# Kernel optimization log

Measured on AMD Instinct MI355X. Metric: run time of the kernel, lower is better.

Reference implementation:

```python
import jax, jax.numpy as jnp
import numpy as np


def _conv1x1(x, w, b):
    # x: [B,Cin,H,W], w: [Cout,Cin], b: [Cout]
    return jnp.einsum('bchw,oc->bohw', x, w) + b[None, :, None, None]


def setup_inputs() -> dict:
    key = jax.random.key(0)
    ks = jax.random.split(key, 9)
    C, Cb = 256, 128
    B, H, W = 8, 32, 32
    s_in = 1.0 / np.sqrt(C)
    s_bn = 1.0 / np.sqrt(Cb)
    return {
        'x': jax.random.normal(ks[0], (B, C, H, W), dtype=jnp.float32),
        'theta_w': jax.random.uniform(ks[1], (Cb, C), jnp.float32, -s_in, s_in),
        'theta_b': jax.random.uniform(ks[2], (Cb,), jnp.float32, -s_in, s_in),
        'phi_w': jax.random.uniform(ks[3], (Cb, C), jnp.float32, -s_in, s_in),
        'phi_b': jax.random.uniform(ks[4], (Cb,), jnp.float32, -s_in, s_in),
        'g_w': jax.random.uniform(ks[5], (Cb, C), jnp.float32, -s_in, s_in),
        'g_b': jax.random.uniform(ks[6], (Cb,), jnp.float32, -s_in, s_in),
        'W_w': jax.random.uniform(ks[7], (C, Cb), jnp.float32, -s_bn, s_bn),
        'W_b': jax.random.uniform(ks[8], (C,), jnp.float32, -s_bn, s_bn),
    }


def reference(x, theta_w, theta_b, phi_w, phi_b, g_w, g_b, W_w, W_b):
    B, C, H, Wd = x.shape
    Cb = theta_w.shape[0]
    theta = _conv1x1(x, theta_w, theta_b).reshape(-1, Cb)      # [N, Cb] (row-major, as torch)
    phi = _conv1x1(x, phi_w, phi_b).reshape(Cb, -1)            # [Cb, N]
    g = _conv1x1(x, g_w, g_b).reshape(-1, Cb)                  # [N, Cb]
    attn = jax.nn.softmax(theta @ phi, axis=1)                 # [N, N] global attention
    out = (attn @ g).reshape(B, -1, H, Wd)                     # [B, Cb, H, W]
    return _conv1x1(out, W_w, W_b) + x
```

## Files before the change

kernel.cpp:

```cpp
#include <hip/hip_runtime.h>

typedef unsigned short u16;
typedef __attribute__((ext_vector_type(8))) short short8;
typedef __attribute__((ext_vector_type(4))) float f32x4;

__device__ __forceinline__ u16 f2bf(float f){
  union { float f; unsigned u; } v; v.f = f;
  unsigned u = v.u;
  u += 0x7fffu + ((u >> 16) & 1u);
  return (u16)(u >> 16);
}
__device__ __forceinline__ float bf2f(u16 h){
  union { unsigned u; float f; } v; v.u = ((unsigned)h) << 16;
  return v.f;
}

__global__ __launch_bounds__(256) void wcast_kernel(
    const float* __restrict__ tw, const float* __restrict__ pw,
    const float* __restrict__ gw, u16* __restrict__ Wall)
{
  int i = blockIdx.x*256 + threadIdx.x;
  const float* src = (i < 8192) ? tw : (i < 16384) ? pw : gw;
  int off = (i & 8191) * 4;
  float4 v = *(const float4*)(src + off);
  ushort4 o;
  o.x = f2bf(v.x); o.y = f2bf(v.y); o.z = f2bf(v.z); o.w = f2bf(v.w);
  *(ushort4*)(Wall + (size_t)i*4) = o;
}

__global__ __launch_bounds__(256) void xcast_kernel(
    const float* __restrict__ x, u16* __restrict__ XT)
{
  __shared__ float tile[64][69];
  const int b = blockIdx.z, c0 = blockIdx.y*64, hw0 = blockIdx.x*64;
  const int t = threadIdx.x;
  {
    int r = t >> 2, cs = (t & 3) * 16;
    const float* s = x + (size_t)(b*256 + c0 + r)*1024 + hw0 + cs;
    #pragma unroll
    for (int i=0;i<4;i++)
      *(float4*)&tile[r][cs + i*4] = *(const float4*)(s + i*4);
  }
  __syncthreads();
  {
    int hr = t >> 2, cc = (t & 3) * 16;
    __align__(16) u16 tmp[16];
    #pragma unroll
    for (int i=0;i<16;i++) tmp[i] = f2bf(tile[cc + i][hr]);
    u16* d = XT + (size_t)(b*1024 + hw0 + hr)*256 + c0 + cc;
    *(uint4*)d     = *(uint4*)&tmp[0];
    *(uint4*)(d+8) = *(uint4*)&tmp[8];
  }
}

__global__ __launch_bounds__(256, 2) void proj_mfma_kernel(
    const u16* __restrict__ XT, const u16* __restrict__ Wall,
    const float* __restrict__ tb, const float* __restrict__ pb,
    const float* __restrict__ gb,
    u16* __restrict__ T, u16* __restrict__ PHI, u16* __restrict__ G)
{
  __shared__ __align__(16) u16 Ws[128][136];
  __shared__ __align__(16) u16 Xs[128][136];
  const int proj = blockIdx.x, qg = blockIdx.y;
  const int b = qg >> 3, hw0 = (qg & 7) * 128;
  const int q0 = qg * 128;
  const u16* Wsrc = Wall + (size_t)proj * 32768;
  const float* bias = (proj==0) ? tb : (proj==1) ? pb : gb;
  u16* out          = (proj==0) ? T  : (proj==1) ? PHI : G;
  const int t = threadIdx.x;
  const int wave = t >> 6, lane = t & 63;
  const int quad = lane >> 4, n16 = lane & 15;

  f32x4 acc[8][2];
  #pragma unroll
  for (int mt=0;mt<8;mt++)
    #pragma unroll
    for (int nt=0;nt<2;nt++){ f32x4 z = {0.f,0.f,0.f,0.f}; acc[mt][nt] = z; }

  for (int c0 = 0; c0 < 256; c0 += 128){
    __syncthreads();
    {
      int row = t >> 1, cb = (t & 1) * 64;
      const u16* s1 = Wsrc + (size_t)row*256 + c0 + cb;
      #pragma unroll
      for (int i=0;i<8;i++)
        *(uint4*)&Ws[row][cb + i*8] = *(const uint4*)(s1 + i*8);
      const u16* s2 = XT + (size_t)(q0 + row)*256 + c0 + cb;
      #pragma unroll
      for (int i=0;i<8;i++)
        *(uint4*)&Xs[row][cb + i*8] = *(const uint4*)(s2 + i*8);
    }
    __syncthreads();
    #pragma unroll
    for (int kc=0; kc<4; kc++){
      short8 xf[2];
      #pragma unroll
      for (int nt=0;nt<2;nt++)
        xf[nt] = *(const short8*)&Xs[wave*32 + nt*16 + n16][kc*32 + quad*8];
      #pragma unroll
      for (int mt=0;mt<8;mt++){
        short8 wf = *(const short8*)&Ws[mt*16 + n16][kc*32 + quad*8];
        #pragma unroll
        for (int nt=0;nt<2;nt++)
          acc[mt][nt] = __builtin_amdgcn_mfma_f32_16x16x32_bf16(wf, xf[nt], acc[mt][nt], 0, 0, 0);
      }
    }
  }
  #pragma unroll
  for (int mt=0;mt<8;mt++){
    float4 bv = *(const float4*)&bias[mt*16 + quad*4];
    float bb[4] = {bv.x, bv.y, bv.z, bv.w};
    #pragma unroll
    for (int nt=0;nt<2;nt++)
      #pragma unroll
      for (int r=0;r<4;r++)
        out[(size_t)b*131072 + (size_t)(mt*16 + quad*4 + r)*1024
            + hw0 + wave*32 + nt*16 + n16] = f2bf(acc[mt][nt][r] + bb[r]);
  }
}

__global__ __launch_bounds__(256) void transpose_bf_kernel(
    const u16* __restrict__ src, u16* __restrict__ dst, int R, int C)
{
  __shared__ u16 tile[64][72];
  const int t = threadIdx.x;
  const int c0 = blockIdx.x*64, r0 = blockIdx.y*64;
  {
    int rr = t >> 2, cs = (t & 3) * 16;
    const u16* s = src + (size_t)(r0+rr)*C + c0 + cs;
    uint4 a0 = *(const uint4*)s;
    uint4 a1 = *(const uint4*)(s+8);
    *(uint4*)&tile[rr][cs]   = a0;
    *(uint4*)&tile[rr][cs+8] = a1;
  }
  __syncthreads();
  {
    int cc = t >> 2, rs = (t & 3) * 16;
    __align__(16) u16 tmp[16];
    #pragma unroll
    for (int i=0;i<16;i++) tmp[i] = tile[rs+i][cc];
    u16* d = dst + (size_t)(c0+cc)*R + r0 + rs;
    *(uint4*)d     = *(uint4*)&tmp[0];
    *(uint4*)(d+8) = *(uint4*)&tmp[8];
  }
}

__global__ __launch_bounds__(256, 2) void attn_kernel(
    const u16* __restrict__ Tq, const u16* __restrict__ Kk,
    const u16* __restrict__ Vt, u16* __restrict__ Opart,
    float* __restrict__ lpart)
{
  __shared__ __align__(16) u16 Ks[64][136];
  __shared__ __align__(16) u16 Vs[128][72];
  __shared__ __align__(16) u16 Pall[4][4608];

  const int t = threadIdx.x;
  const int wave = t >> 6, lane = t & 63;
  const int quad = lane >> 4, n16 = lane & 15;
  const int s  = blockIdx.x & 15;
  const int qg = blockIdx.x >> 4;
  const int q0 = qg*256 + wave*64;
  u16* Pw = Pall[wave];
  u16*   Os = Opart + (size_t)s * 1048576;
  float* ls = lpart + (size_t)s * 8192;

  short8 qa[4][4];
  #pragma unroll
  for (int mt=0;mt<4;mt++)
    #pragma unroll
    for (int kc=0;kc<4;kc++)
      qa[mt][kc] = *(const short8*)(Tq + (size_t)(q0 + mt*16 + n16)*128 + kc*32 + quad*8);

  f32x4 o[4][8];
  float lp[4];
  #pragma unroll
  for (int mt=0;mt<4;mt++){
    #pragma unroll
    for (int dt=0;dt<8;dt++){ f32x4 z = {0.f,0.f,0.f,0.f}; o[mt][dt] = z; }
    lp[mt] = 0.f;
  }

  const int krow = t >> 2, kcs = (t & 3) * 32;
  const int vrow = t >> 1, vcs = (t & 1) * 32;
  const int wmask = n16 & 14;

  for (int kt = s*8; kt < s*8 + 8; kt++){
    const int key0 = kt * 64;
    __syncthreads();
    #pragma unroll
    for (int i=0;i<4;i++)
      *(uint4*)&Ks[krow][kcs + i*8] =
        *(const uint4*)(Kk + (size_t)(key0 + krow)*128 + kcs + i*8);
    #pragma unroll
    for (int i=0;i<4;i++)
      *(uint4*)&Vs[vrow][vcs + i*8] =
        *(const uint4*)(Vt + (size_t)vrow*8192 + key0 + vcs + i*8);
    __syncthreads();

    #pragma unroll
    for (int ntk=0; ntk<4; ntk++){
      short8 kf[4];
      #pragma unroll
      for (int kc=0;kc<4;kc++)
        kf[kc] = *(const short8*)&Ks[ntk*16 + n16][kc*32 + quad*8];
      #pragma unroll
      for (int mtq=0;mtq<4;mtq++){
        f32x4 sa = {0.f,0.f,0.f,0.f};
        #pragma unroll
        for (int kc=0;kc<4;kc++)
          sa = __builtin_amdgcn_mfma_f32_16x16x32_bf16(kf[kc], qa[mtq][kc], sa, 0, 0, 0);
        u16 pb[4];
        #pragma unroll
        for (int r=0;r<4;r++){
          float pe = exp2f(sa[r] * 1.4426950408889634f);
          lp[mtq] += pe;
          pb[r] = f2bf(pe);
        }
        uint2 pk;
        pk.x = ((unsigned)pb[1] << 16) | pb[0];
        pk.y = ((unsigned)pb[3] << 16) | pb[2];
        *(uint2*)(Pw + (mtq*16 + n16)*72 + (((ntk*4 + quad) ^ wmask) << 2)) = pk;
      }
    }

    __builtin_amdgcn_s_waitcnt(0xC07F);

    #pragma unroll
    for (int kb=0; kb<2; kb++){
      short8 pf[4];
      #pragma unroll
      for (int mtq=0;mtq<4;mtq++)
        pf[mtq] = *(const short8*)(Pw + (mtq*16 + n16)*72 + (((kb*8 + quad*2) ^ wmask) << 2));
      #pragma unroll
      for (int dt=0; dt<8; dt++){
        short8 vfd = *(const short8*)&Vs[dt*16 + n16][kb*32 + quad*8];
        #pragma unroll
        for (int mtq=0;mtq<4;mtq++)
          o[mtq][dt] = __builtin_amdgcn_mfma_f32_16x16x32_bf16(pf[mtq], vfd, o[mtq][dt], 0, 0, 0);
      }
    }
  }

  float l[4];
  #pragma unroll
  for (int mt=0;mt<4;mt++){
    float v = lp[mt];
    v += __shfl_xor(v, 16, 64);
    v += __shfl_xor(v, 32, 64);
    l[mt] = v;
  }

  #pragma unroll
  for (int mt=0;mt<4;mt++){
    #pragma unroll
    for (int r=0;r<4;r++){
      __align__(16) u16 tmp[8];
      #pragma unroll
      for (int dt=0;dt<8;dt++) tmp[dt] = f2bf(o[mt][dt][r]);
      *(uint4*)(Os + (size_t)(q0 + mt*16 + quad*4 + r)*128 + n16*8) = *(uint4*)tmp;
    }
    if (lane < 16)
      ls[q0 + mt*16 + lane] = l[mt];
  }
}

__global__ __launch_bounds__(256) void merge_o_kernel(
    const u16* __restrict__ Opart, const float* __restrict__ lpart, int S,
    u16* __restrict__ OmT)
{
  __shared__ u16 Tm[64][136];
  __shared__ float lrow[64];
  const int t = threadIdx.x;
  const int row0 = blockIdx.x * 64;
  const int b  = row0 >> 10;
  const int j0 = (row0 >> 3) & 127;

  if (t < 64){
    float v = 0.f;
    for (int sp=0; sp<S; sp++) v += lpart[sp*8192 + row0 + t];
    lrow[t] = 1.0f / v;
  }

  const int rl = t >> 2;
  const int cb = (t & 3) * 32;
  float acc[32];
  #pragma unroll
  for (int j=0;j<32;j++) acc[j] = 0.f;
  for (int sp=0; sp<S; sp++){
    const u16* p = Opart + (size_t)sp*1048576 + (size_t)(row0 + rl)*128 + cb;
    #pragma unroll
    for (int q=0;q<4;q++){
      ushort4 v = *(const ushort4*)(p + q*8);
      ushort4 w = *(const ushort4*)(p + q*8 + 4);
      acc[q*8+0] += bf2f(v.x); acc[q*8+1] += bf2f(v.y);
      acc[q*8+2] += bf2f(v.z); acc[q*8+3] += bf2f(v.w);
      acc[q*8+4] += bf2f(w.x); acc[q*8+5] += bf2f(w.y);
      acc[q*8+6] += bf2f(w.z); acc[q*8+7] += bf2f(w.w);
    }
  }
  __syncthreads();
  const float inv = lrow[rl];
  #pragma unroll
  for (int j=0;j<32;j++){
    int cp = cb + j;
    int ch = (cp & 7)*16 + (cp >> 3);
    Tm[rl][ch] = f2bf(acc[j] * inv);
  }
  __syncthreads();
  {
    const int hwhi = t >> 5;
    const int chb  = (t & 31) * 4;
    #pragma unroll
    for (int c=0;c<4;c++){
      int ch = chb + c;
      __align__(16) u16 tmp[8];
      #pragma unroll
      for (int jl=0;jl<8;jl++) tmp[jl] = Tm[jl*8 + hwhi][ch];
      *(uint4*)(OmT + (size_t)(b*1024 + hwhi*128 + ch)*128 + j0) = *(uint4*)tmp;
    }
  }
}

__global__ __launch_bounds__(256, 2) void final_mfma_kernel(
    const float* __restrict__ Ww, const float* __restrict__ Wb,
    const u16* __restrict__ OmT, const float* __restrict__ x,
    float* __restrict__ outp)
{
  __shared__ __align__(16) u16 Ws[64][136];
  __shared__ __align__(16) u16 Os[128][136];
  const int co0 = blockIdx.x * 64, qg = blockIdx.y;
  const int b = qg >> 3, hw0 = (qg & 7) * 128;
  const int q0 = qg * 128;
  const int t = threadIdx.x;
  const int wave = t >> 6, lane = t & 63;
  const int quad = lane >> 4, n16 = lane & 15;

  {
    int row = t >> 2, cbf = (t & 3) * 32;
    const float* sw = Ww + (size_t)(co0 + row)*128 + cbf;
    #pragma unroll
    for (int i=0;i<8;i++){
      float4 v = *(const float4*)(sw + i*4);
      u16* d = &Ws[row][cbf + i*4];
      d[0]=f2bf(v.x); d[1]=f2bf(v.y); d[2]=f2bf(v.z); d[3]=f2bf(v.w);
    }
  }
  {
    int row = t >> 1, cb = (t & 1) * 64;
    const u16* so = OmT + (size_t)(q0 + row)*128 + cb;
    #pragma unroll
    for (int i=0;i<8;i++)
      *(uint4*)&Os[row][cb + i*8] = *(const uint4*)(so + i*8);
  }
  __syncthreads();

  f32x4 acc[4][2];
  #pragma unroll
  for (int mt=0;mt<4;mt++)
    #pragma unroll
    for (int nt=0;nt<2;nt++){ f32x4 z = {0.f,0.f,0.f,0.f}; acc[mt][nt] = z; }

  #pragma unroll
  for (int kc=0; kc<4; kc++){
    short8 xf[2];
    #pragma unroll
    for (int nt=0;nt<2;nt++)
      xf[nt] = *(const short8*)&Os[wave*32 + nt*16 + n16][kc*32 + quad*8];
    #pragma unroll
    for (int mt=0;mt<4;mt++){
      short8 wf = *(const short8*)&Ws[mt*16 + n16][kc*32 + quad*8];
      #pragma unroll
      for (int nt=0;nt<2;nt++)
        acc[mt][nt] = __builtin_amdgcn_mfma_f32_16x16x32_bf16(wf, xf[nt], acc[mt][nt], 0, 0, 0);
    }
  }

  #pragma unroll
  for (int mt=0;mt<4;mt++){
    float4 bv = *(const float4*)&Wb[co0 + mt*16 + quad*4];
    float bb[4] = {bv.x, bv.y, bv.z, bv.w};
    #pragma unroll
    for (int nt=0;nt<2;nt++)
      #pragma unroll
      for (int r=0;r<4;r++){
        size_t idx = (size_t)b*262144 + (size_t)(co0 + mt*16 + quad*4 + r)*1024
                   + hw0 + wave*32 + nt*16 + n16;
        outp[idx] = acc[mt][nt][r] + bb[r] + x[idx];
      }
  }
}

extern "C" void kernel_launch(void* const* d_in, const int* in_sizes, int n_in,
                              void* d_out, int out_size, void* d_ws, size_t ws_size,
                              hipStream_t stream)
{
  (void)in_sizes; (void)n_in; (void)out_size; (void)ws_size;
  const float* x  = (const float*)d_in[0];
  const float* tw = (const float*)d_in[1];
  const float* tb = (const float*)d_in[2];
  const float* pw = (const float*)d_in[3];
  const float* pb = (const float*)d_in[4];
  const float* gw = (const float*)d_in[5];
  const float* gb = (const float*)d_in[6];
  const float* Ww = (const float*)d_in[7];
  const float* Wb = (const float*)d_in[8];
  float* outp = (float*)d_out;

  char* ws = (char*)d_ws;
  const size_t MB = 1u << 20;
  u16*   Tbf   = (u16*)(ws);
  u16*   PHIbf = (u16*)(ws + 2*MB);
  u16*   Gbf   = (u16*)(ws + 4*MB);
  u16*   Kbf   = (u16*)(ws + 6*MB);
  u16*   VTbf  = (u16*)(ws + 8*MB);
  u16*   Opart = (u16*)(ws + 10*MB);
  u16*   XT    = (u16*)(ws + 10*MB);
  u16*   Wall  = (u16*)(ws + 14*MB);
  float* lpart = (float*)(ws + 2*MB);
  u16*   OmT   = (u16*)(ws + 4*MB);

  wcast_kernel<<<dim3(96), 256, 0, stream>>>(tw, pw, gw, Wall);
  xcast_kernel<<<dim3(16, 4, 8), 256, 0, stream>>>(x, XT);
  proj_mfma_kernel<<<dim3(3, 64), 256, 0, stream>>>(XT, Wall, tb, pb, gb,
                                                    Tbf, PHIbf, Gbf);
  transpose_bf_kernel<<<dim3(128, 2), 256, 0, stream>>>(PHIbf, Kbf, 128, 8192);
  transpose_bf_kernel<<<dim3(2, 128), 256, 0, stream>>>(Gbf, VTbf, 8192, 128);
  attn_kernel<<<dim3(512), 256, 0, stream>>>(Tbf, Kbf, VTbf, Opart, lpart);
  merge_o_kernel<<<dim3(128), 256, 0, stream>>>(Opart, lpart, 16, OmT);
  final_mfma_kernel<<<dim3(4, 64), 256, 0, stream>>>(Ww, Wb, OmT, x, outp);
}
```

Measured before the change: 187.9 us.

## Fuse weight cast into projection, prefetch K/V tiles, fold log2e, split merge finer

Removes the separate weight-cast kernel; the projection kernel now reads fp32 weights and converts them to bf16 while filling shared memory. It also folds the log2(e) factor into theta so the attention loop can call the raw exp2 builtin. The attention kernel gains register double-buffered K/V prefetch, so global loads overlap MFMA compute, and raises wave priority around the PV MFMAs. Merge now uses 32-row blocks to launch twice as many workgroups. Risks include higher register pressure in the attention kernel, extra fp32 weight reads per block, and a slightly different rounding point from scaling theta before the bf16 cast.

```diff
diff --git a/kernel.cpp b/kernel.cpp
--- a/kernel.cpp
+++ b/kernel.cpp
@@ -15,19 +15,6 @@
   return v.f;
 }
 
-__global__ __launch_bounds__(256) void wcast_kernel(
-    const float* __restrict__ tw, const float* __restrict__ pw,
-    const float* __restrict__ gw, u16* __restrict__ Wall)
-{
-  int i = blockIdx.x*256 + threadIdx.x;
-  const float* src = (i < 8192) ? tw : (i < 16384) ? pw : gw;
-  int off = (i & 8191) * 4;
-  float4 v = *(const float4*)(src + off);
-  ushort4 o;
-  o.x = f2bf(v.x); o.y = f2bf(v.y); o.z = f2bf(v.z); o.w = f2bf(v.w);
-  *(ushort4*)(Wall + (size_t)i*4) = o;
-}
-
 __global__ __launch_bounds__(256) void xcast_kernel(
     const float* __restrict__ x, u16* __restrict__ XT)
 {
@@ -54,7 +41,9 @@
 }
 
 __global__ __launch_bounds__(256, 2) void proj_mfma_kernel(
-    const u16* __restrict__ XT, const u16* __restrict__ Wall,
+    const u16* __restrict__ XT,
+    const float* __restrict__ tw, const float* __restrict__ pw,
+    const float* __restrict__ gw,
     const float* __restrict__ tb, const float* __restrict__ pb,
     const float* __restrict__ gb,
     u16* __restrict__ T, u16* __restrict__ PHI, u16* __restrict__ G)
@@ -64,9 +53,10 @@
   const int proj = blockIdx.x, qg = blockIdx.y;
   const int b = qg >> 3, hw0 = (qg & 7) * 128;
   const int q0 = qg * 128;
-  const u16* Wsrc = Wall + (size_t)proj * 32768;
+  const float* Wf   = (proj==0) ? tw : (proj==1) ? pw : gw;
   const float* bias = (proj==0) ? tb : (proj==1) ? pb : gb;
   u16* out          = (proj==0) ? T  : (proj==1) ? PHI : G;
+  const float scale = (proj==0) ? 1.4426950408889634f : 1.0f;
   const int t = threadIdx.x;
   const int wave = t >> 6, lane = t & 63;
   const int quad = lane >> 4, n16 = lane & 15;
@@ -81,10 +71,13 @@
     __syncthreads();
     {
       int row = t >> 1, cb = (t & 1) * 64;
-      const u16* s1 = Wsrc + (size_t)row*256 + c0 + cb;
-      #pragma unroll
-      for (int i=0;i<8;i++)
-        *(uint4*)&Ws[row][cb + i*8] = *(const uint4*)(s1 + i*8);
+      const float* s1 = Wf + (size_t)row*256 + c0 + cb;
+      #pragma unroll
+      for (int i=0;i<16;i++){
+        float4 v = *(const float4*)(s1 + i*4);
+        u16* d = &Ws[row][cb + i*4];
+        d[0]=f2bf(v.x); d[1]=f2bf(v.y); d[2]=f2bf(v.z); d[3]=f2bf(v.w);
+      }
       const u16* s2 = XT + (size_t)(q0 + row)*256 + c0 + cb;
       #pragma unroll
       for (int i=0;i<8;i++)
@@ -115,7 +108,7 @@
       #pragma unroll
       for (int r=0;r<4;r++)
         out[(size_t)b*131072 + (size_t)(mt*16 + quad*4 + r)*1024
-            + hw0 + wave*32 + nt*16 + n16] = f2bf(acc[mt][nt][r] + bb[r]);
+            + hw0 + wave*32 + nt*16 + n16] = f2bf((acc[mt][nt][r] + bb[r]) * scale);
   }
 }
 
@@ -184,19 +177,21 @@
   const int vrow = t >> 1, vcs = (t & 1) * 32;
   const int wmask = n16 & 14;
 
-  for (int kt = s*8; kt < s*8 + 8; kt++){
-    const int key0 = kt * 64;
-    __syncthreads();
+  auto LOAD = [&](uint4* kr, uint4* vr, int key0){
     #pragma unroll
     for (int i=0;i<4;i++)
-      *(uint4*)&Ks[krow][kcs + i*8] =
-        *(const uint4*)(Kk + (size_t)(key0 + krow)*128 + kcs + i*8);
+      kr[i] = *(const uint4*)(Kk + (size_t)(key0 + krow)*128 + kcs + i*8);
     #pragma unroll
     for (int i=0;i<4;i++)
-      *(uint4*)&Vs[vrow][vcs + i*8] =
-        *(const uint4*)(Vt + (size_t)vrow*8192 + key0 + vcs + i*8);
-    __syncthreads();
-
+      vr[i] = *(const uint4*)(Vt + (size_t)vrow*8192 + key0 + vcs + i*8);
+  };
+  auto WRITE = [&](const uint4* kr, const uint4* vr){
+    #pragma unroll
+    for (int i=0;i<4;i++) *(uint4*)&Ks[krow][kcs + i*8] = kr[i];
+    #pragma unroll
+    for (int i=0;i<4;i++) *(uint4*)&Vs[vrow][vcs + i*8] = vr[i];
+  };
+  auto COMPUTE = [&](){
     #pragma unroll
     for (int ntk=0; ntk<4; ntk++){
       short8 kf[4];
@@ -212,7 +207,7 @@
         u16 pb[4];
         #pragma unroll
         for (int r=0;r<4;r++){
-          float pe = exp2f(sa[r] * 1.4426950408889634f);
+          float pe = __builtin_amdgcn_exp2f(sa[r]);
           lp[mtq] += pe;
           pb[r] = f2bf(pe);
         }
@@ -222,15 +217,14 @@
         *(uint2*)(Pw + (mtq*16 + n16)*72 + (((ntk*4 + quad) ^ wmask) << 2)) = pk;
       }
     }
-
     __builtin_amdgcn_s_waitcnt(0xC07F);
-
     #pragma unroll
     for (int kb=0; kb<2; kb++){
       short8 pf[4];
       #pragma unroll
       for (int mtq=0;mtq<4;mtq++)
         pf[mtq] = *(const short8*)(Pw + (mtq*16 + n16)*72 + (((kb*8 + quad*2) ^ wmask) << 2));
+      __builtin_amdgcn_s_setprio(1);
       #pragma unroll
       for (int dt=0; dt<8; dt++){
         short8 vfd = *(const short8*)&Vs[dt*16 + n16][kb*32 + quad*8];
@@ -238,7 +232,24 @@
         for (int mtq=0;mtq<4;mtq++)
           o[mtq][dt] = __builtin_amdgcn_mfma_f32_16x16x32_bf16(pf[mtq], vfd, o[mtq][dt], 0, 0, 0);
       }
-    }
+      __builtin_amdgcn_s_setprio(0);
+    }
+  };
+
+  uint4 ka[4], va[4], kb_[4], vb_[4];
+  LOAD(ka, va, s*512);
+  #pragma unroll 1
+  for (int it=0; it<4; it++){
+    __syncthreads();
+    WRITE(ka, va);
+    LOAD(kb_, vb_, s*512 + (2*it+1)*64);
+    __syncthreads();
+    COMPUTE();
+    __syncthreads();
+    WRITE(kb_, vb_);
+    if (it < 3) LOAD(ka, va, s*512 + (2*it+2)*64);
+    __syncthreads();
+    COMPUTE();
   }
 
   float l[4];
@@ -268,28 +279,28 @@
     const u16* __restrict__ Opart, const float* __restrict__ lpart, int S,
     u16* __restrict__ OmT)
 {
-  __shared__ u16 Tm[64][136];
-  __shared__ float lrow[64];
-  const int t = threadIdx.x;
-  const int row0 = blockIdx.x * 64;
+  __shared__ u16 Tm[32][136];
+  __shared__ float lrow[32];
+  const int t = threadIdx.x;
+  const int row0 = blockIdx.x * 32;
   const int b  = row0 >> 10;
   const int j0 = (row0 >> 3) & 127;
 
-  if (t < 64){
+  if (t < 32){
     float v = 0.f;
     for (int sp=0; sp<S; sp++) v += lpart[sp*8192 + row0 + t];
     lrow[t] = 1.0f / v;
   }
 
-  const int rl = t >> 2;
-  const int cb = (t & 3) * 32;
-  float acc[32];
-  #pragma unroll
-  for (int j=0;j<32;j++) acc[j] = 0.f;
+  const int rl = t >> 3;
+  const int cb = (t & 7) * 16;
+  float acc[16];
+  #pragma unroll
+  for (int j=0;j<16;j++) acc[j] = 0.f;
   for (int sp=0; sp<S; sp++){
     const u16* p = Opart + (size_t)sp*1048576 + (size_t)(row0 + rl)*128 + cb;
     #pragma unroll
-    for (int q=0;q<4;q++){
+    for (int q=0;q<2;q++){
       ushort4 v = *(const ushort4*)(p + q*8);
       ushort4 w = *(const ushort4*)(p + q*8 + 4);
       acc[q*8+0] += bf2f(v.x); acc[q*8+1] += bf2f(v.y);
@@ -301,7 +312,7 @@
   __syncthreads();
   const float inv = lrow[rl];
   #pragma unroll
-  for (int j=0;j<32;j++){
+  for (int j=0;j<16;j++){
     int cp = cb + j;
     int ch = (cp & 7)*16 + (cp >> 3);
     Tm[rl][ch] = f2bf(acc[j] * inv);
@@ -313,10 +324,10 @@
     #pragma unroll
     for (int c=0;c<4;c++){
       int ch = chb + c;
-      __align__(16) u16 tmp[8];
-      #pragma unroll
-      for (int jl=0;jl<8;jl++) tmp[jl] = Tm[jl*8 + hwhi][ch];
-      *(uint4*)(OmT + (size_t)(b*1024 + hwhi*128 + ch)*128 + j0) = *(uint4*)tmp;
+      __align__(8) u16 tmp[4];
+      #pragma unroll
+      for (int jl=0;jl<4;jl++) tmp[jl] = Tm[jl*8 + hwhi][ch];
+      *(uint2*)(OmT + (size_t)(b*1024 + hwhi*128 + ch)*128 + j0) = *(uint2*)tmp;
     }
   }
 }
@@ -415,17 +426,15 @@
   u16*   VTbf  = (u16*)(ws + 8*MB);
   u16*   Opart = (u16*)(ws + 10*MB);
   u16*   XT    = (u16*)(ws + 10*MB);
-  u16*   Wall  = (u16*)(ws + 14*MB);
   float* lpart = (float*)(ws + 2*MB);
   u16*   OmT   = (u16*)(ws + 4*MB);
 
-  wcast_kernel<<<dim3(96), 256, 0, stream>>>(tw, pw, gw, Wall);
   xcast_kernel<<<dim3(16, 4, 8), 256, 0, stream>>>(x, XT);
-  proj_mfma_kernel<<<dim3(3, 64), 256, 0, stream>>>(XT, Wall, tb, pb, gb,
+  proj_mfma_kernel<<<dim3(3, 64), 256, 0, stream>>>(XT, tw, pw, gw, tb, pb, gb,
                                                     Tbf, PHIbf, Gbf);
   transpose_bf_kernel<<<dim3(128, 2), 256, 0, stream>>>(PHIbf, Kbf, 128, 8192);
   transpose_bf_kernel<<<dim3(2, 128), 256, 0, stream>>>(Gbf, VTbf, 8192, 128);
   attn_kernel<<<dim3(512), 256, 0, stream>>>(Tbf, Kbf, VTbf, Opart, lpart);
-  merge_o_kernel<<<dim3(128), 256, 0, stream>>>(Opart, lpart, 16, OmT);
+  merge_o_kernel<<<dim3(256), 256, 0, stream>>>(Opart, lpart, 16, OmT);
   final_mfma_kernel<<<dim3(4, 64), 256, 0, stream>>>(Ww, Wb, OmT, x, outp);
 }
```

After: 273.8 us. 45.7% more time.
